# Kernel optimization log

Measured on AMD Instinct MI355X. Metric: run time of the kernel, lower is better.

## Reference

```python
import jax, jax.numpy as jnp
import numpy as np

N, E, D_IN, H, D_EF = 20000, 320000, 128, 128, 32

def gcn_conv(x, src, dst, W, b, n):
    # PyG GCNConv: add self-loops, symmetric normalization, then linear transform
    xw = x @ W                                    # [N, out]
    loop = jnp.arange(n)
    s = jnp.concatenate([src, loop])
    d = jnp.concatenate([dst, loop])
    deg = jax.ops.segment_sum(jnp.ones_like(s, dtype=xw.dtype), d, num_segments=n)
    dinv = jnp.where(deg > 0, jax.lax.rsqrt(jnp.maximum(deg, 1e-12)), 0.0)
    norm = dinv[s] * dinv[d]                      # [E+N]
    msg = xw[s] * norm[:, None]
    out = jax.ops.segment_sum(msg, d, num_segments=n)
    return out + b

def lstm_layer(seq, wih, whh, bih, bhh):
    # seq: [T, in]; PyTorch gate order i, f, g, o
    h_dim = whh.shape[1]
    gx = seq @ wih.T + (bih + bhh)                # precompute input contribution [T, 4H]
    def step(carry, gxt):
        h, c = carry
        g = gxt + h @ whh.T
        i, f, gg, o = jnp.split(g, 4, axis=-1)
        c = jax.nn.sigmoid(f) * c + jax.nn.sigmoid(i) * jnp.tanh(gg)
        h = jax.nn.sigmoid(o) * jnp.tanh(c)
        return (h, c), h
    h0 = jnp.zeros((h_dim,), seq.dtype)
    (hT, cT), hs = jax.lax.scan(step, (h0, h0), gx)
    return hs, hT, cT

def setup_inputs() -> dict:
    key = jax.random.key(0)
    ks = jax.random.split(key, 20)
    s = 0.05
    inp = {
        'x': jax.random.normal(ks[0], (N, D_IN), jnp.float32),
        'edge_index': jax.random.randint(ks[1], (2, E), 0, N, dtype=jnp.int64),
        'edge_features': jax.random.normal(ks[2], (E, D_EF), jnp.float32),
        'W1': jax.random.normal(ks[3], (D_IN, H), jnp.float32) * s,
        'b1': jnp.zeros((H,), jnp.float32),
        'W2': jax.random.normal(ks[4], (H, H), jnp.float32) * s,
        'b2': jnp.zeros((H,), jnp.float32),
        'wih0': jax.random.normal(ks[5], (4 * H, H), jnp.float32) * s,
        'whh0': jax.random.normal(ks[6], (4 * H, H), jnp.float32) * s,
        'bih0': jnp.zeros((4 * H,), jnp.float32),
        'bhh0': jnp.zeros((4 * H,), jnp.float32),
        'wih1': jax.random.normal(ks[7], (4 * H, H), jnp.float32) * s,
        'whh1': jax.random.normal(ks[8], (4 * H, H), jnp.float32) * s,
        'bih1': jnp.zeros((4 * H,), jnp.float32),
        'bhh1': jnp.zeros((4 * H,), jnp.float32),
        'eW': jax.random.normal(ks[9], (D_EF, H), jnp.float32) * s,
        'eb': jnp.zeros((H,), jnp.float32),
        'cW': jax.random.normal(ks[10], (3 * H, 1), jnp.float32) * s,
        'cb': jnp.zeros((1,), jnp.float32),
    }
    return inp

def reference(x, edge_index, edge_features, W1, b1, W2, b2,
              wih0, whh0, bih0, bhh0, wih1, whh1, bih1, bhh1,
              eW, eb, cW, cb):
    src_i, dst_i = edge_index[0], edge_index[1]
    h = jax.nn.relu(gcn_conv(x, src_i, dst_i, W1, b1, N))   # dropout is identity (p used in eval / p=0)
    h = gcn_conv(h, src_i, dst_i, W2, b2, N)                # [N, H]
    # LSTM: batch=1, seq_len=N (x.unsqueeze(0), batch_first=True), 2 layers
    hs0, h0T, c0T = lstm_layer(h, wih0, whh0, bih0, bhh0)
    hs1, h1T, c1T = lstm_layer(hs0, wih1, whh1, bih1, bhh1)
    lstm_out = hs1                                          # [N, H]
    edge_emb = edge_features @ eW + eb                      # [E, H]
    src = lstm_out[src_i]
    dst = lstm_out[dst_i]
    combined = jnp.concatenate([src, dst, edge_emb], axis=-1)  # [E, 3H]
    edge_pred = combined @ cW + cb                          # [E, 1]
    hn = jnp.stack([h0T, h1T])[:, None, :]                  # [num_layers, 1, H]
    cn = jnp.stack([c0T, c1T])[:, None, :]
    return (edge_pred, hn, cn, src, dst)
```

## Files before the change

kernel.cpp:

```cpp
#include <hip/hip_runtime.h>
#include <cstdint>
#include <cstddef>


typedef __attribute__((ext_vector_type(8))) short short8x;
typedef __attribute__((ext_vector_type(4))) float f32x4;

static __device__ __forceinline__ unsigned short f2bf(float x) {
  union { float f; unsigned u; } v; v.f = x;
  unsigned r = (v.u + 0x7fffu + ((v.u >> 16) & 1u)) >> 16;
  return (unsigned short)r;
}
static __device__ __forceinline__ float bf2f(unsigned short s) {
  union { unsigned u; float f; } v; v.u = ((unsigned)s) << 16; return v.f;
}
static __device__ __forceinline__ float sigm(float x) {
  return 1.f / (1.f + __expf(-x));
}
static __device__ __forceinline__ float tanh_(float x) {
  float e = __expf(2.f * x);
  return 1.f - 2.f / (e + 1.f);
}

__global__ __launch_bounds__(256) void k_deg(const int* __restrict__ ei,
                                             int* __restrict__ deg, int E) {
  int e = blockIdx.x * 256 + threadIdx.x;
  if (e < E) atomicAdd(&deg[ei[E + e]], 1);
}

__global__ __launch_bounds__(256) void k_dinv(const int* __restrict__ deg,
                                              float* __restrict__ dinv, int n) {
  int i = blockIdx.x * 256 + threadIdx.x;
  if (i < n) dinv[i] = rsqrtf((float)(deg[i] + 1));
}

__global__ __launch_bounds__(256) void k_gemm(
    const float* __restrict__ A, const float* __restrict__ B, void* __restrict__ C,
    int M, int N, int bnmajor, const float* __restrict__ bias0,
    const float* __restrict__ bias1, int obf16) {
  __shared__ float As[32][128];
  __shared__ float Bs[128][68];
  const int t  = threadIdx.x;
  const int m0 = blockIdx.x * 32;
  const int n0 = blockIdx.y * 64;

  for (int i = t; i < 1024; i += 256) {
    int r = i >> 5, c4 = i & 31;
    *(float4*)&As[r][c4 * 4] = *(const float4*)(A + (size_t)(m0 + r) * 128 + c4 * 4);
  }
  if (!bnmajor) {
    for (int i = t; i < 2048; i += 256) {
      int r = i >> 4, c4 = i & 15;
      float4 v = *(const float4*)(B + (size_t)r * N + n0 + c4 * 4);
      *(float4*)&Bs[r][c4 * 4] = v;
    }
  } else {
    for (int i = t; i < 2048; i += 256) {
      int n = i >> 5, k4 = i & 31;
      float4 v = *(const float4*)(B + (size_t)(n0 + n) * 128 + k4 * 4);
      Bs[k4 * 4 + 0][n] = v.x; Bs[k4 * 4 + 1][n] = v.y;
      Bs[k4 * 4 + 2][n] = v.z; Bs[k4 * 4 + 3][n] = v.w;
    }
  }
  __syncthreads();

  const int nl = t & 31, mg = t >> 5;
  float acc[4][2] = {};
  for (int k = 0; k < 128; ++k) {
    float b0 = Bs[k][nl], b1 = Bs[k][nl + 32];
    float a0 = As[mg * 4 + 0][k], a1 = As[mg * 4 + 1][k];
    float a2 = As[mg * 4 + 2][k], a3 = As[mg * 4 + 3][k];
    acc[0][0] += a0 * b0; acc[0][1] += a0 * b1;
    acc[1][0] += a1 * b0; acc[1][1] += a1 * b1;
    acc[2][0] += a2 * b0; acc[2][1] += a2 * b1;
    acc[3][0] += a3 * b0; acc[3][1] += a3 * b1;
  }
  float bv0 = 0.f, bv1 = 0.f;
  if (bias0) { bv0 += bias0[n0 + nl]; bv1 += bias0[n0 + nl + 32]; }
  if (bias1) { bv0 += bias1[n0 + nl]; bv1 += bias1[n0 + nl + 32]; }
#pragma unroll
  for (int i = 0; i < 4; ++i) {
    size_t row = (size_t)(m0 + mg * 4 + i) * N;
    float v0 = acc[i][0] + bv0, v1 = acc[i][1] + bv1;
    if (obf16) {
      ((unsigned short*)C)[row + n0 + nl]      = f2bf(v0);
      ((unsigned short*)C)[row + n0 + nl + 32] = f2bf(v1);
    } else {
      ((float*)C)[row + n0 + nl]      = v0;
      ((float*)C)[row + n0 + nl + 32] = v1;
    }
  }
}

__global__ __launch_bounds__(256) void k_scaleinit(float* __restrict__ y,
                                                   float* __restrict__ acc,
                                                   const float* __restrict__ dinv,
                                                   int total4) {
  int i = blockIdx.x * 256 + threadIdx.x;
  if (i >= total4) return;
  float s = dinv[i >> 5];
  float4 v = ((const float4*)y)[i];
  v.x *= s; v.y *= s; v.z *= s; v.w *= s;
  ((float4*)y)[i] = v;
  ((float4*)acc)[i] = v;
}

__global__ __launch_bounds__(256) void k_scatter(const float* __restrict__ y,
                                                 float* __restrict__ acc,
                                                 const int* __restrict__ ei, int E) {
  int g = blockIdx.x * 256 + threadIdx.x;
  int e = g >> 5, q = g & 31;
  if (e >= E) return;
  int s = ei[e], d = ei[E + e];
  float4 v = *(const float4*)(y + (size_t)s * 128 + q * 4);
  float* p = acc + (size_t)d * 128 + q * 4;
  atomicAdd(p + 0, v.x); atomicAdd(p + 1, v.y);
  atomicAdd(p + 2, v.z); atomicAdd(p + 3, v.w);
}

__global__ __launch_bounds__(256) void k_finish(const float* __restrict__ acc,
                                                float* __restrict__ outb,
                                                const float* __restrict__ dinv,
                                                const float* __restrict__ bias,
                                                int total4, int relu) {
  int i = blockIdx.x * 256 + threadIdx.x;
  if (i >= total4) return;
  float s = dinv[i >> 5];
  float4 v = ((const float4*)acc)[i];
  float4 b = *(const float4*)(bias + (i & 31) * 4);
  v.x = v.x * s + b.x; v.y = v.y * s + b.y;
  v.z = v.z * s + b.z; v.w = v.w * s + b.w;
  if (relu) {
    v.x = fmaxf(v.x, 0.f); v.y = fmaxf(v.y, 0.f);
    v.z = fmaxf(v.z, 0.f); v.w = fmaxf(v.w, 0.f);
  }
  ((float4*)outb)[i] = v;
}

#define MFMA16(a, b, c) __builtin_amdgcn_mfma_f32_16x16x32_bf16((a), (b), (c), 0, 0, 0)

__global__ __launch_bounds__(512, 2) void k_lstm(
    const unsigned short* __restrict__ gx0b,
    const float* __restrict__ whh0, const float* __restrict__ wih1,
    const float* __restrict__ whh1, const float* __restrict__ bih1,
    const float* __restrict__ bhh1, float* __restrict__ hs1,
    float* __restrict__ hncn, int T) {
  __shared__ __align__(16) unsigned short h0buf[128];
  __shared__ __align__(16) unsigned short h1buf[128];
  __shared__ float gbuf[512];
  __shared__ __align__(16) unsigned short gxlds[32 * 512];
  __shared__ __align__(16) float hslds[32 * 128];

  const int tid  = threadIdx.x;
  const int lane = tid & 63;
  const int wave = tid >> 6;
  const int col  = lane & 15;
  const int kg   = lane >> 4;

  short8x fr0[4][4], fr1[4][4], fr2[4][4];
  {
    const int nbase = wave * 64 + col;
#pragma unroll
    for (int nt = 0; nt < 4; ++nt) {
#pragma unroll
      for (int kt = 0; kt < 4; ++kt) {
        const int n  = nbase + nt * 16;
        const int k0 = kt * 32 + kg * 8;
        const float* p0 = whh0 + (size_t)n * 128 + k0;
        const float* p1 = wih1 + (size_t)n * 128 + k0;
        const float* p2 = whh1 + (size_t)n * 128 + k0;
        short8x a, b, c;
#pragma unroll
        for (int j = 0; j < 8; ++j) {
          a[j] = (short)f2bf(p0[j]);
          b[j] = (short)f2bf(p1[j]);
          c[j] = (short)f2bf(p2[j]);
        }
        fr0[nt][kt] = a; fr1[nt][kt] = b; fr2[nt][kt] = c;
      }
    }
  }

  float c0 = 0.f, c1 = 0.f, h0f = 0.f, h1f = 0.f;
  float b2i = 0.f, b2f = 0.f, b2g = 0.f, b2o = 0.f;
  if (tid < 128) {
    b2i = bih1[tid]       + bhh1[tid];
    b2f = bih1[tid + 128] + bhh1[tid + 128];
    b2g = bih1[tid + 256] + bhh1[tid + 256];
    b2o = bih1[tid + 384] + bhh1[tid + 384];
    h0buf[tid] = 0; h1buf[tid] = 0;
  }
  __syncthreads();

  for (int t = 0; t < T; ++t) {
    if ((t & 31) == 0) {
      const short8x* src = (const short8x*)(gx0b + (size_t)t * 512);
      short8x* dst = (short8x*)gxlds;
#pragma unroll
      for (int r = 0; r < 4; ++r) {
        int i = tid + 512 * r;
        dst[i] = src[i];
      }
    }

    f32x4 acc0 = {0.f, 0.f, 0.f, 0.f}, acc1 = acc0, acc2 = acc0, acc3 = acc0;
#pragma unroll
    for (int kt = 0; kt < 4; ++kt) {
      short8x a = *(const short8x*)(h0buf + kt * 32 + kg * 8);
      acc0 = MFMA16(a, fr0[0][kt], acc0);
      acc1 = MFMA16(a, fr0[1][kt], acc1);
      acc2 = MFMA16(a, fr0[2][kt], acc2);
      acc3 = MFMA16(a, fr0[3][kt], acc3);
    }
    if (lane < 16) {
      gbuf[wave * 64 + 0  + lane] = acc0[0];
      gbuf[wave * 64 + 16 + lane] = acc1[0];
      gbuf[wave * 64 + 32 + lane] = acc2[0];
      gbuf[wave * 64 + 48 + lane] = acc3[0];
    }
    __syncthreads();

    if (tid < 128) {
      const unsigned short* gx = gxlds + (size_t)(t & 31) * 512 + tid;
      float gi = bf2f(gx[0])   + gbuf[tid];
      float gf = bf2f(gx[128]) + gbuf[tid + 128];
      float gg = bf2f(gx[256]) + gbuf[tid + 256];
      float go = bf2f(gx[384]) + gbuf[tid + 384];
      float iv = sigm(gi), fv = sigm(gf), gv = tanh_(gg), ov = sigm(go);
      c0 = fv * c0 + iv * gv;
      h0f = ov * tanh_(c0);
      h0buf[tid] = f2bf(h0f);
    }
    __syncthreads();

    acc0 = (f32x4){0.f, 0.f, 0.f, 0.f}; acc1 = acc0; acc2 = acc0; acc3 = acc0;
#pragma unroll
    for (int kt = 0; kt < 4; ++kt) {
      short8x a = *(const short8x*)(h0buf + kt * 32 + kg * 8);
      acc0 = MFMA16(a, fr1[0][kt], acc0);
      acc1 = MFMA16(a, fr1[1][kt], acc1);
      acc2 = MFMA16(a, fr1[2][kt], acc2);
      acc3 = MFMA16(a, fr1[3][kt], acc3);
    }
#pragma unroll
    for (int kt = 0; kt < 4; ++kt) {
      short8x a = *(const short8x*)(h1buf + kt * 32 + kg * 8);
      acc0 = MFMA16(a, fr2[0][kt], acc0);
      acc1 = MFMA16(a, fr2[1][kt], acc1);
      acc2 = MFMA16(a, fr2[2][kt], acc2);
      acc3 = MFMA16(a, fr2[3][kt], acc3);
    }
    if (lane < 16) {
      gbuf[wave * 64 + 0  + lane] = acc0[0];
      gbuf[wave * 64 + 16 + lane] = acc1[0];
      gbuf[wave * 64 + 32 + lane] = acc2[0];
      gbuf[wave * 64 + 48 + lane] = acc3[0];
    }
    __syncthreads();

    if (tid < 128) {
      float gi = gbuf[tid]       + b2i;
      float gf = gbuf[tid + 128] + b2f;
      float gg = gbuf[tid + 256] + b2g;
      float go = gbuf[tid + 384] + b2o;
      float iv = sigm(gi), fv = sigm(gf), gv = tanh_(gg), ov = sigm(go);
      c1 = fv * c1 + iv * gv;
      h1f = ov * tanh_(c1);
      h1buf[tid] = f2bf(h1f);
      hslds[(t & 31) * 128 + tid] = h1f;
    }
    __syncthreads();

    if ((t & 31) == 31 || t == T - 1) {
      int t0 = t & ~31;
      int cnt = ((t & 31) + 1) * 32;
      float4* dst = (float4*)(hs1 + (size_t)t0 * 128);
      for (int i = tid; i < cnt; i += 512) dst[i] = ((const float4*)hslds)[i];
    }
  }

  if (tid < 128) {
    hncn[tid]       = h0f;
    hncn[128 + tid] = h1f;
    hncn[256 + tid] = c0;
    hncn[384 + tid] = c1;
  }
}

__global__ __launch_bounds__(256) void k_edge(
    const float* __restrict__ S, const int* __restrict__ ei,
    const float* __restrict__ ef, const float* __restrict__ eW,
    const float* __restrict__ eb, const float* __restrict__ cW,
    const float* __restrict__ cb, float* __restrict__ out, int E) {
  const int lane = threadIdx.x & 63;
  const int gw   = (blockIdx.x * 256 + threadIdx.x) >> 6;
  const int nw   = gridDim.x * 4;
  const size_t so = (size_t)E + 512;
  const size_t doff = so + (size_t)E * 128;

  const float cs0 = cW[2 * lane], cs1 = cW[2 * lane + 1];
  const float cd0 = cW[128 + 2 * lane], cd1 = cW[128 + 2 * lane + 1];
  const float ce0 = cW[256 + lane], ce1 = cW[320 + lane];
  const float eb0 = eb[lane], eb1 = eb[lane + 64];
  const float cbv = cb[0];

  for (int e = gw; e < E; e += nw) {
    int s = ei[e], d = ei[E + e];
    float2 vs = *(const float2*)(S + (size_t)s * 128 + 2 * lane);
    float2 vd = *(const float2*)(S + (size_t)d * 128 + 2 * lane);
    *(float2*)(out + so + (size_t)e * 128 + 2 * lane) = vs;
    *(float2*)(out + doff + (size_t)e * 128 + 2 * lane) = vd;

    float a0 = eb0, a1 = eb1;
    const float* efr = ef + (size_t)e * 32;
#pragma unroll
    for (int k = 0; k < 32; ++k) {
      float x = efr[k];
      a0 += x * eW[k * 128 + lane];
      a1 += x * eW[k * 128 + 64 + lane];
    }
    float p = vs.x * cs0 + vs.y * cs1 + vd.x * cd0 + vd.y * cd1 + a0 * ce0 + a1 * ce1;
#pragma unroll
    for (int m = 32; m; m >>= 1) p += __shfl_xor(p, m, 64);
    if (lane == 0) out[e] = p + cbv;
  }
}

extern "C" void kernel_launch(void* const* d_in, const int* in_sizes, int n_in,
                              void* d_out, int out_size, void* d_ws, size_t ws_size,
                              hipStream_t stream) {
  const float* x    = (const float*)d_in[0];
  const int*   ei   = (const int*)d_in[1];
  const float* ef   = (const float*)d_in[2];
  const float* W1   = (const float*)d_in[3];
  const float* b1   = (const float*)d_in[4];
  const float* W2   = (const float*)d_in[5];
  const float* b2   = (const float*)d_in[6];
  const float* wih0 = (const float*)d_in[7];
  const float* whh0 = (const float*)d_in[8];
  const float* bih0 = (const float*)d_in[9];
  const float* bhh0 = (const float*)d_in[10];
  const float* wih1 = (const float*)d_in[11];
  const float* whh1 = (const float*)d_in[12];
  const float* bih1 = (const float*)d_in[13];
  const float* bhh1 = (const float*)d_in[14];
  const float* eW   = (const float*)d_in[15];
  const float* eb   = (const float*)d_in[16];
  const float* cW   = (const float*)d_in[17];
  const float* cb   = (const float*)d_in[18];

  const int nN = in_sizes[0] / 128;
  const int E  = in_sizes[1] / 2;

  char* ws = (char*)d_ws;
  float* dinv          = (float*)ws;
  int*   deg           = (int*)(ws + 81920);
  float* buf1          = (float*)(ws + 163840);
  float* buf2          = buf1 + (size_t)nN * 128;
  float* buf3          = buf2 + (size_t)nN * 128;
  unsigned short* G    = (unsigned short*)(buf3 + (size_t)nN * 128);
  float* S             = (float*)(G + (size_t)nN * 512);
  float* out           = (float*)d_out;

  const int total4 = nN * 32;
  const int gElem  = (total4 + 255) / 256;
  const dim3 g128(nN / 32, 2);
  const dim3 g512(nN / 32, 8);

  hipMemsetAsync(deg, 0, nN * sizeof(int), stream);
  k_deg<<<(E + 255) / 256, 256, 0, stream>>>(ei, deg, E);
  k_dinv<<<(nN + 255) / 256, 256, 0, stream>>>(deg, dinv, nN);

  k_gemm<<<g128, 256, 0, stream>>>(x, W1, buf1, nN, 128, 0, nullptr, nullptr, 0);
  k_scaleinit<<<gElem, 256, 0, stream>>>(buf1, buf2, dinv, total4);
  k_scatter<<<(E * 32 + 255) / 256, 256, 0, stream>>>(buf1, buf2, ei, E);
  k_finish<<<gElem, 256, 0, stream>>>(buf2, buf3, dinv, b1, total4, 1);

  k_gemm<<<g128, 256, 0, stream>>>(buf3, W2, buf1, nN, 128, 0, nullptr, nullptr, 0);
  k_scaleinit<<<gElem, 256, 0, stream>>>(buf1, buf2, dinv, total4);
  k_scatter<<<(E * 32 + 255) / 256, 256, 0, stream>>>(buf1, buf2, ei, E);
  k_finish<<<gElem, 256, 0, stream>>>(buf2, buf3, dinv, b2, total4, 0);

  k_gemm<<<g512, 256, 0, stream>>>(buf3, wih0, G, nN, 512, 1, bih0, bhh0, 1);

  k_lstm<<<1, 512, 0, stream>>>(G, whh0, wih1, whh1, bih1, bhh1, S, out + (size_t)E, nN);

  k_edge<<<2048, 256, 0, stream>>>(S, ei, ef, eW, eb, cW, cb, out, E);
}
```

Measured before the change: 34.88 ms.

## Skew LSTM layers into one barrier per step with gate-interleaved weights

Restructures the two-layer LSTM recurrence so that each step runs layer 0 at time t and layer 1 at time t-1 at the same moment. Each wave owns 16 hidden columns across all four gates, so gate values stay in registers and the gbuf round trips plus three of the four barriers per step go away. The gx GEMM output is rewritten in a gate-interleaved layout so each thread can prefetch its four gate inputs for the next step with a single load. Fast-divide intrinsics replace the exact divisions in sigmoid and tanh. In exchange there is one extra loop iteration, redundant MFMAs on the padding steps, and hs1 is now written directly per step rather than staged in shared memory.

```diff
diff --git a/kernel.cpp b/kernel.cpp
--- a/kernel.cpp
+++ b/kernel.cpp
@@ -5,6 +5,7 @@
 
 typedef __attribute__((ext_vector_type(8))) short short8x;
 typedef __attribute__((ext_vector_type(4))) float f32x4;
+typedef __attribute__((ext_vector_type(4))) unsigned short ushort4x;
 
 static __device__ __forceinline__ unsigned short f2bf(float x) {
   union { float f; unsigned u; } v; v.f = x;
@@ -15,11 +16,11 @@
   union { unsigned u; float f; } v; v.u = ((unsigned)s) << 16; return v.f;
 }
 static __device__ __forceinline__ float sigm(float x) {
-  return 1.f / (1.f + __expf(-x));
+  return __fdividef(1.f, 1.f + __expf(-x));
 }
 static __device__ __forceinline__ float tanh_(float x) {
   float e = __expf(2.f * x);
-  return 1.f - 2.f / (e + 1.f);
+  return 1.f - __fdividef(2.f, e + 1.f);
 }
 
 __global__ __launch_bounds__(256) void k_deg(const int* __restrict__ ei,
@@ -78,16 +79,19 @@
   float bv0 = 0.f, bv1 = 0.f;
   if (bias0) { bv0 += bias0[n0 + nl]; bv1 += bias0[n0 + nl + 32]; }
   if (bias1) { bv0 += bias1[n0 + nl]; bv1 += bias1[n0 + nl + 32]; }
+  const int c0i = n0 + nl, c1i = n0 + nl + 32;
+  const int p0i = ((c0i & 127) << 2) | (c0i >> 7);
+  const int p1i = ((c1i & 127) << 2) | (c1i >> 7);
 #pragma unroll
   for (int i = 0; i < 4; ++i) {
     size_t row = (size_t)(m0 + mg * 4 + i) * N;
     float v0 = acc[i][0] + bv0, v1 = acc[i][1] + bv1;
     if (obf16) {
-      ((unsigned short*)C)[row + n0 + nl]      = f2bf(v0);
-      ((unsigned short*)C)[row + n0 + nl + 32] = f2bf(v1);
+      ((unsigned short*)C)[row + p0i] = f2bf(v0);
+      ((unsigned short*)C)[row + p1i] = f2bf(v1);
     } else {
-      ((float*)C)[row + n0 + nl]      = v0;
-      ((float*)C)[row + n0 + nl + 32] = v1;
+      ((float*)C)[row + c0i] = v0;
+      ((float*)C)[row + c1i] = v1;
     }
   }
 }
@@ -140,150 +144,118 @@
 #define MFMA16(a, b, c) __builtin_amdgcn_mfma_f32_16x16x32_bf16((a), (b), (c), 0, 0, 0)
 
 __global__ __launch_bounds__(512, 2) void k_lstm(
-    const unsigned short* __restrict__ gx0b,
+    const unsigned short* __restrict__ G,
     const float* __restrict__ whh0, const float* __restrict__ wih1,
     const float* __restrict__ whh1, const float* __restrict__ bih1,
     const float* __restrict__ bhh1, float* __restrict__ hs1,
     float* __restrict__ hncn, int T) {
-  __shared__ __align__(16) unsigned short h0buf[128];
-  __shared__ __align__(16) unsigned short h1buf[128];
-  __shared__ float gbuf[512];
-  __shared__ __align__(16) unsigned short gxlds[32 * 512];
-  __shared__ __align__(16) float hslds[32 * 128];
+  __shared__ __align__(16) unsigned short h0buf[2][128];
+  __shared__ __align__(16) unsigned short h1buf[2][128];
 
   const int tid  = threadIdx.x;
   const int lane = tid & 63;
   const int wave = tid >> 6;
   const int col  = lane & 15;
   const int kg   = lane >> 4;
-
-  short8x fr0[4][4], fr1[4][4], fr2[4][4];
-  {
-    const int nbase = wave * 64 + col;
-#pragma unroll
-    for (int nt = 0; nt < 4; ++nt) {
-#pragma unroll
-      for (int kt = 0; kt < 4; ++kt) {
-        const int n  = nbase + nt * 16;
-        const int k0 = kt * 32 + kg * 8;
-        const float* p0 = whh0 + (size_t)n * 128 + k0;
-        const float* p1 = wih1 + (size_t)n * 128 + k0;
-        const float* p2 = whh1 + (size_t)n * 128 + k0;
-        short8x a, b, c;
-#pragma unroll
-        for (int j = 0; j < 8; ++j) {
-          a[j] = (short)f2bf(p0[j]);
-          b[j] = (short)f2bf(p1[j]);
-          c[j] = (short)f2bf(p2[j]);
-        }
-        fr0[nt][kt] = a; fr1[nt][kt] = b; fr2[nt][kt] = c;
+  const int myc  = wave * 16 + col;
+
+  short8x B1[4][4], B2[4][8];
+#pragma unroll
+  for (int g = 0; g < 4; ++g) {
+    const float* p0 = whh0 + (size_t)(g * 128 + myc) * 128 + kg * 8;
+    const float* p1 = wih1 + (size_t)(g * 128 + myc) * 128 + kg * 8;
+    const float* p2 = whh1 + (size_t)(g * 128 + myc) * 128 + kg * 8;
+#pragma unroll
+    for (int kt = 0; kt < 4; ++kt) {
+      short8x v0, v1, v2;
+#pragma unroll
+      for (int j = 0; j < 8; ++j) {
+        v0[j] = (short)f2bf(p0[kt * 32 + j]);
+        v1[j] = (short)f2bf(p1[kt * 32 + j]);
+        v2[j] = (short)f2bf(p2[kt * 32 + j]);
       }
-    }
-  }
-
+      B1[g][kt] = v0; B2[g][kt] = v1; B2[g][kt + 4] = v2;
+    }
+  }
+  const float b2i = bih1[myc]       + bhh1[myc];
+  const float b2f = bih1[myc + 128] + bhh1[myc + 128];
+  const float b2g = bih1[myc + 256] + bhh1[myc + 256];
+  const float b2o = bih1[myc + 384] + bhh1[myc + 384];
+
+  if (tid < 128) {
+    h0buf[0][tid] = 0; h0buf[1][tid] = 0;
+    h1buf[0][tid] = 0; h1buf[1][tid] = 0;
+  }
   float c0 = 0.f, c1 = 0.f, h0f = 0.f, h1f = 0.f;
-  float b2i = 0.f, b2f = 0.f, b2g = 0.f, b2o = 0.f;
-  if (tid < 128) {
-    b2i = bih1[tid]       + bhh1[tid];
-    b2f = bih1[tid + 128] + bhh1[tid + 128];
-    b2g = bih1[tid + 256] + bhh1[tid + 256];
-    b2o = bih1[tid + 384] + bhh1[tid + 384];
-    h0buf[tid] = 0; h1buf[tid] = 0;
-  }
+
+  ushort4x gxn = *(const ushort4x*)(G + (size_t)0 * 512 + myc * 4);
   __syncthreads();
 
-  for (int t = 0; t < T; ++t) {
-    if ((t & 31) == 0) {
-      const short8x* src = (const short8x*)(gx0b + (size_t)t * 512);
-      short8x* dst = (short8x*)gxlds;
-#pragma unroll
-      for (int r = 0; r < 4; ++r) {
-        int i = tid + 512 * r;
-        dst[i] = src[i];
+  for (int t = 0; t <= T; ++t) {
+    const int p = t & 1;
+
+    ushort4x gxc = gxn;
+    {
+      int tn = t + 1; if (tn >= T) tn = T - 1;
+      gxn = *(const ushort4x*)(G + (size_t)tn * 512 + myc * 4);
+    }
+
+    f32x4 z = {0.f, 0.f, 0.f, 0.f};
+    f32x4 a1i = z, a1f = z, a1g = z, a1o = z;
+    f32x4 a2i = z, a2f = z, a2g = z, a2o = z;
+#pragma unroll
+    for (int kt = 0; kt < 4; ++kt) {
+      short8x a = *(const short8x*)(&h0buf[p][kt * 32 + kg * 8]);
+      a1i = MFMA16(a, B1[0][kt], a1i);
+      a1f = MFMA16(a, B1[1][kt], a1f);
+      a1g = MFMA16(a, B1[2][kt], a1g);
+      a1o = MFMA16(a, B1[3][kt], a1o);
+      a2i = MFMA16(a, B2[0][kt], a2i);
+      a2f = MFMA16(a, B2[1][kt], a2f);
+      a2g = MFMA16(a, B2[2][kt], a2g);
+      a2o = MFMA16(a, B2[3][kt], a2o);
+    }
+#pragma unroll
+    for (int kt = 0; kt < 4; ++kt) {
+      short8x a = *(const short8x*)(&h1buf[p][kt * 32 + kg * 8]);
+      a2i = MFMA16(a, B2[0][kt + 4], a2i);
+      a2f = MFMA16(a, B2[1][kt + 4], a2f);
+      a2g = MFMA16(a, B2[2][kt + 4], a2g);
+      a2o = MFMA16(a, B2[3][kt + 4], a2o);
+    }
+
+    if (t < T) {
+      float gi = bf2f(gxc[0]) + a1i[0];
+      float gf = bf2f(gxc[1]) + a1f[0];
+      float gg = bf2f(gxc[2]) + a1g[0];
+      float go = bf2f(gxc[3]) + a1o[0];
+      c0 = sigm(gf) * c0 + sigm(gi) * tanh_(gg);
+      h0f = sigm(go) * tanh_(c0);
+      if (lane < 16) h0buf[p ^ 1][myc] = f2bf(h0f);
+    }
+    if (t > 0) {
+      float gi = a2i[0] + b2i;
+      float gf = a2f[0] + b2f;
+      float gg = a2g[0] + b2g;
+      float go = a2o[0] + b2o;
+      c1 = sigm(gf) * c1 + sigm(gi) * tanh_(gg);
+      h1f = sigm(go) * tanh_(c1);
+      if (lane < 16) {
+        h1buf[p ^ 1][myc] = f2bf(h1f);
+        hs1[(size_t)(t - 1) * 128 + myc] = h1f;
       }
     }
 
-    f32x4 acc0 = {0.f, 0.f, 0.f, 0.f}, acc1 = acc0, acc2 = acc0, acc3 = acc0;
-#pragma unroll
-    for (int kt = 0; kt < 4; ++kt) {
-      short8x a = *(const short8x*)(h0buf + kt * 32 + kg * 8);
-      acc0 = MFMA16(a, fr0[0][kt], acc0);
-      acc1 = MFMA16(a, fr0[1][kt], acc1);
-      acc2 = MFMA16(a, fr0[2][kt], acc2);
-      acc3 = MFMA16(a, fr0[3][kt], acc3);
-    }
-    if (lane < 16) {
-      gbuf[wave * 64 + 0  + lane] = acc0[0];
-      gbuf[wave * 64 + 16 + lane] = acc1[0];
-      gbuf[wave * 64 + 32 + lane] = acc2[0];
-      gbuf[wave * 64 + 48 + lane] = acc3[0];
-    }
-    __syncthreads();
-
-    if (tid < 128) {
-      const unsigned short* gx = gxlds + (size_t)(t & 31) * 512 + tid;
-      float gi = bf2f(gx[0])   + gbuf[tid];
-      float gf = bf2f(gx[128]) + gbuf[tid + 128];
-      float gg = bf2f(gx[256]) + gbuf[tid + 256];
-      float go = bf2f(gx[384]) + gbuf[tid + 384];
-      float iv = sigm(gi), fv = sigm(gf), gv = tanh_(gg), ov = sigm(go);
-      c0 = fv * c0 + iv * gv;
-      h0f = ov * tanh_(c0);
-      h0buf[tid] = f2bf(h0f);
-    }
-    __syncthreads();
-
-    acc0 = (f32x4){0.f, 0.f, 0.f, 0.f}; acc1 = acc0; acc2 = acc0; acc3 = acc0;
-#pragma unroll
-    for (int kt = 0; kt < 4; ++kt) {
-      short8x a = *(const short8x*)(h0buf + kt * 32 + kg * 8);
-      acc0 = MFMA16(a, fr1[0][kt], acc0);
-      acc1 = MFMA16(a, fr1[1][kt], acc1);
-      acc2 = MFMA16(a, fr1[2][kt], acc2);
-      acc3 = MFMA16(a, fr1[3][kt], acc3);
-    }
-#pragma unroll
-    for (int kt = 0; kt < 4; ++kt) {
-      short8x a = *(const short8x*)(h1buf + kt * 32 + kg * 8);
-      acc0 = MFMA16(a, fr2[0][kt], acc0);
-      acc1 = MFMA16(a, fr2[1][kt], acc1);
-      acc2 = MFMA16(a, fr2[2][kt], acc2);
-      acc3 = MFMA16(a, fr2[3][kt], acc3);
-    }
-    if (lane < 16) {
-      gbuf[wave * 64 + 0  + lane] = acc0[0];
-      gbuf[wave * 64 + 16 + lane] = acc1[0];
-      gbuf[wave * 64 + 32 + lane] = acc2[0];
-      gbuf[wave * 64 + 48 + lane] = acc3[0];
-    }
-    __syncthreads();
-
-    if (tid < 128) {
-      float gi = gbuf[tid]       + b2i;
-      float gf = gbuf[tid + 128] + b2f;
-      float gg = gbuf[tid + 256] + b2g;
-      float go = gbuf[tid + 384] + b2o;
-      float iv = sigm(gi), fv = sigm(gf), gv = tanh_(gg), ov = sigm(go);
-      c1 = fv * c1 + iv * gv;
-      h1f = ov * tanh_(c1);
-      h1buf[tid] = f2bf(h1f);
-      hslds[(t & 31) * 128 + tid] = h1f;
-    }
-    __syncthreads();
-
-    if ((t & 31) == 31 || t == T - 1) {
-      int t0 = t & ~31;
-      int cnt = ((t & 31) + 1) * 32;
-      float4* dst = (float4*)(hs1 + (size_t)t0 * 128);
-      for (int i = tid; i < cnt; i += 512) dst[i] = ((const float4*)hslds)[i];
-    }
-  }
-
-  if (tid < 128) {
-    hncn[tid]       = h0f;
-    hncn[128 + tid] = h1f;
-    hncn[256 + tid] = c0;
-    hncn[384 + tid] = c1;
+    asm volatile("s_waitcnt lgkmcnt(0)" ::: "memory");
+    __builtin_amdgcn_s_barrier();
+    asm volatile("" ::: "memory");
+  }
+
+  if (lane < 16) {
+    hncn[myc]       = h0f;
+    hncn[128 + myc] = h1f;
+    hncn[256 + myc] = c0;
+    hncn[384 + myc] = c1;
   }
 }
 
```

Result: faster. 30.35 ms (-13.0%).
